# Kernel tuning notes

Hardware: AMD Instinct MI355X
Metric: run time of the kernel (lower is better)

## Reference

```python
import jax, jax.numpy as jnp
import numpy as np

N_REP = 8      # N: repeated gelu(LN(linear)) blocks
M_LAYERS = 4   # M: transformer encoder layers
SEQ = 100
D = 4
FF = 2048      # PyTorch TransformerEncoderLayer default dim_feedforward
H = 4          # nhead; head_dim = 1


def _ln(x, g, b, axes):
    m = jnp.mean(x, axis=axes, keepdims=True)
    v = jnp.var(x, axis=axes, keepdims=True)
    return (x - m) / jnp.sqrt(v + 1e-5) * g + b


def _encoder_layer(x, Win, bi, Wout, bout, W1, b1, W2, b2, g1, be1, g2, be2):
    # x: [S, Nb, D] with S = batch_size (batch_first=False!), Nb = 100
    S, Nb, E = x.shape
    qkv = x @ Win.T + bi                      # [S, Nb, 3D]
    q, k, v = jnp.split(qkv, 3, axis=-1)
    qh = q.reshape(S, Nb, H, E // H)          # head_dim = 1, scale 1/sqrt(1)=1
    kh = k.reshape(S, Nb, H, E // H)
    vh = v.reshape(S, Nb, H, E // H)
    scores = jnp.einsum('snhd,tnhd->nhst', qh, kh)   # [Nb, H, S, S]
    attn = jax.nn.softmax(scores, axis=-1)
    o = jnp.einsum('nhst,tnhd->snhd', attn, vh).reshape(S, Nb, E)
    o = o @ Wout.T + bout
    x = _ln(x + o, g1, be1, (-1,))            # post-norm (norm_first=False)
    f = jax.nn.relu(x @ W1.T + b1) @ W2.T + b2
    return _ln(x + f, g2, be2, (-1,))


def setup_inputs() -> dict:
    key = jax.random.key(0)
    ks = jax.random.split(key, 24)
    B = 256
    d = {}
    d['x'] = jax.random.normal(ks[0], (B, SEQ, D), dtype=jnp.float32)
    # conv1: kernel_size=1, 1->1 channel -> scalar affine
    d['conv_w'] = jax.random.normal(ks[1], (), dtype=jnp.float32) * 0.5 + 1.0
    d['conv_b'] = jax.random.normal(ks[2], (), dtype=jnp.float32) * 0.1
    # shared 4x4 linear (self.liner) and LayerNorm([100,4])
    d['Wl'] = jax.random.normal(ks[3], (D, D), dtype=jnp.float32) * 0.5
    d['bl'] = jax.random.normal(ks[4], (D,), dtype=jnp.float32) * 0.1
    d['ln_g'] = jnp.ones((SEQ, D), dtype=jnp.float32)
    d['ln_b'] = jnp.zeros((SEQ, D), dtype=jnp.float32)
    # transformer encoder params, stacked over M layers
    s = 0.3
    d['Win'] = jax.random.normal(ks[5], (M_LAYERS, 3 * D, D), dtype=jnp.float32) * s
    d['bi'] = jax.random.normal(ks[6], (M_LAYERS, 3 * D), dtype=jnp.float32) * 0.05
    d['Wout'] = jax.random.normal(ks[7], (M_LAYERS, D, D), dtype=jnp.float32) * s
    d['bout'] = jax.random.normal(ks[8], (M_LAYERS, D), dtype=jnp.float32) * 0.05
    d['W1'] = jax.random.normal(ks[9], (M_LAYERS, FF, D), dtype=jnp.float32) * 0.05
    d['b1'] = jax.random.normal(ks[10], (M_LAYERS, FF), dtype=jnp.float32) * 0.05
    d['W2'] = jax.random.normal(ks[11], (M_LAYERS, D, FF), dtype=jnp.float32) * 0.02
    d['b2'] = jax.random.normal(ks[12], (M_LAYERS, D), dtype=jnp.float32) * 0.05
    d['g1'] = jnp.ones((M_LAYERS, D), dtype=jnp.float32)
    d['be1'] = jnp.zeros((M_LAYERS, D), dtype=jnp.float32)
    d['g2'] = jnp.ones((M_LAYERS, D), dtype=jnp.float32)
    d['be2'] = jnp.zeros((M_LAYERS, D), dtype=jnp.float32)
    return d


def reference(x, conv_w, conv_b, Wl, bl, ln_g, ln_b,
              Win, bi, Wout, bout, W1, b1, W2, b2, g1, be1, g2, be2):
    # per-channel kernel_size=1 conv == elementwise affine (same scalar for all 4 channels)
    h = x * conv_w + conv_b                   # [B, 100, 4]
    for _ in range(N_REP):
        h = jax.nn.gelu(_ln(h @ Wl.T + bl, ln_g, ln_b, (-2, -1)), approximate=False)
    h = h @ Wl.T + bl
    for i in range(M_LAYERS):
        h = _encoder_layer(h, Win[i], bi[i], Wout[i], bout[i], W1[i], b1[i],
                           W2[i], b2[i], g1[i], be1[i], g2[i], be2[i])
    h = h @ Wl.T + bl
    return jax.nn.softmax(h, axis=2)
```

## Files before the change

kernel.cpp:

```cpp
#include <hip/hip_runtime.h>
#include <math.h>

#define SEQ   100
#define BATCH 256
#define NREP  8
#define FFD   2048
#define RSQRT2 0.70710678118654752440f

typedef __attribute__((ext_vector_type(16))) float fv16;
typedef __attribute__((ext_vector_type(4)))  float fv4;

__device__ __forceinline__ float wsum(float v) {
#pragma unroll
  for (int o = 32; o > 0; o >>= 1) v += __shfl_xor(v, o, 64);
  return v;
}

__global__ __launch_bounds__(256) void k_prep(
    const float* __restrict__ W1, const float* __restrict__ b1,
    const float* __restrict__ W2, float* __restrict__ Wp)
{
  const int id = blockIdx.x * 256 + threadIdx.x;
  const int l = id >> 9, g = id & 511, f0 = g * 4;
  float* dst = Wp + id * 36;
  const float* w1 = W1 + (l * FFD + f0) * 4;
#pragma unroll
  for (int i = 0; i < 16; ++i) dst[i] = w1[i];
  const float* w2 = W2 + l * 4 * FFD;
#pragma unroll
  for (int f = 0; f < 4; ++f)
#pragma unroll
    for (int d = 0; d < 4; ++d) dst[16 + f * 4 + d] = w2[d * FFD + f0 + f];
  const float* bb = b1 + l * FFD + f0;
#pragma unroll
  for (int f = 0; f < 4; ++f) dst[32 + f] = bb[f];
}

__global__ __launch_bounds__(64) void k_stageA(
    const float* __restrict__ x, const float* __restrict__ convw,
    const float* __restrict__ convb, const float* __restrict__ Wl,
    const float* __restrict__ bl, const float* __restrict__ lng,
    const float* __restrict__ lnb, float* __restrict__ XT)
{
  const int b = blockIdx.x;
  const int lane = threadIdx.x;
  const bool act = lane < 50;

  const float cw = convw[0], cb = convb[0];
  float W[4][4], B[4];
#pragma unroll
  for (int j = 0; j < 4; ++j) {
    B[j] = bl[j];
#pragma unroll
    for (int d = 0; d < 4; ++d) W[j][d] = Wl[j * 4 + d];
  }
  float h[2][4] = {{0.f,0.f,0.f,0.f},{0.f,0.f,0.f,0.f}};
  float gg[2][4] = {{0.f}}, eb[2][4] = {{0.f}};
  if (act) {
#pragma unroll
    for (int p = 0; p < 2; ++p) {
      const int r = lane * 2 + p;
      float4 xr = *(const float4*)(x + (b * SEQ + r) * 4);
      h[p][0] = fmaf(xr.x, cw, cb); h[p][1] = fmaf(xr.y, cw, cb);
      h[p][2] = fmaf(xr.z, cw, cb); h[p][3] = fmaf(xr.w, cw, cb);
      float4 gv = *(const float4*)(lng + r * 4);
      float4 bv = *(const float4*)(lnb + r * 4);
      gg[p][0] = gv.x; gg[p][1] = gv.y; gg[p][2] = gv.z; gg[p][3] = gv.w;
      eb[p][0] = bv.x; eb[p][1] = bv.y; eb[p][2] = bv.z; eb[p][3] = bv.w;
    }
  }
  for (int it = 0; it < NREP; ++it) {
    float y[2][4] = {{0.f,0.f,0.f,0.f},{0.f,0.f,0.f,0.f}};
    float s1 = 0.f, s2 = 0.f;
    if (act) {
#pragma unroll
      for (int p = 0; p < 2; ++p)
#pragma unroll
        for (int j = 0; j < 4; ++j) {
          float yy = B[j];
#pragma unroll
          for (int d = 0; d < 4; ++d) yy = fmaf(h[p][d], W[j][d], yy);
          y[p][j] = yy; s1 += yy; s2 = fmaf(yy, yy, s2);
        }
    }
    s1 = wsum(s1); s2 = wsum(s2);
    const float mean = s1 * (1.0f / 400.0f);
    const float var  = s2 * (1.0f / 400.0f) - mean * mean;
    const float rstd = rsqrtf(var + 1e-5f);
    if (act) {
#pragma unroll
      for (int p = 0; p < 2; ++p)
#pragma unroll
        for (int j = 0; j < 4; ++j) {
          float vv = fmaf((y[p][j] - mean) * rstd, gg[p][j], eb[p][j]);
          h[p][j] = 0.5f * vv * (1.0f + erff(vv * RSQRT2));
        }
    }
  }
  if (act) {
#pragma unroll
    for (int p = 0; p < 2; ++p) {
      const int r = lane * 2 + p;
      float yy[4];
#pragma unroll
      for (int j = 0; j < 4; ++j) {
        float a = B[j];
#pragma unroll
        for (int d = 0; d < 4; ++d) a = fmaf(h[p][d], W[j][d], a);
        yy[j] = a;
      }
      *(float4*)(XT + (r * BATCH + b) * 4) =
          make_float4(yy[0], yy[1], yy[2], yy[3]);
    }
  }
}

__global__ __launch_bounds__(1024, 4) void k_layer(
    const float* __restrict__ XTin, float* __restrict__ XTout,
    const float* __restrict__ Wa,  const float* __restrict__ ba,
    const float* __restrict__ Wo,  const float* __restrict__ bo,
    const float* __restrict__ Wpl, const float* __restrict__ b2l,
    const float* __restrict__ g1l, const float* __restrict__ e1l,
    const float* __restrict__ g2l, const float* __restrict__ e2l,
    const float* __restrict__ Wl,  const float* __restrict__ bl,
    float* __restrict__ out, const int last)
{
  const int n      = blockIdx.x;
  const int base_s = blockIdx.y * 128;
  const int t      = threadIdx.x;
  const int lane   = t & 63;
  const int wv     = t >> 6;
  const int ah     = wv & 3;
  const int kq     = wv >> 2;

  __shared__ __align__(16) float2 kv[4][256];
  __shared__ float2 part[4][128][5];
  __shared__ float  osm[4][128];
  __shared__ float  x1s[128][4];
  __shared__ float  pacc[16][128][4];
  __shared__ float2 kred[4][4];

  {
    const int s = t & 255, hh = t >> 8;
    float4 xr = *(const float4*)(XTin + (n * BATCH + s) * 4);
    const float* wk = Wa + (4 + hh) * 4;
    const float* wp = Wa + (8 + hh) * 4;
    float k = ba[4+hh] + xr.x*wk[0] + xr.y*wk[1] + xr.z*wk[2] + xr.w*wk[3];
    float v = ba[8+hh] + xr.x*wp[0] + xr.y*wp[1] + xr.z*wp[2] + xr.w*wp[3];
    kv[hh][s] = make_float2(k, v);
  }
  float q0, q1;
  {
    const float* wq = Wa + ah * 4;
    float4 xa = *(const float4*)(XTin + (n * BATCH + base_s + 2 * lane) * 4);
    float4 xb = *(const float4*)(XTin + (n * BATCH + base_s + 2 * lane + 1) * 4);
    q0 = ba[ah] + xa.x*wq[0] + xa.y*wq[1] + xa.z*wq[2] + xa.w*wq[3];
    q1 = ba[ah] + xb.x*wq[0] + xb.y*wq[1] + xb.z*wq[2] + xb.w*wq[3];
  }
  __syncthreads();

  {
    float k = kv[ah][kq * 64 + lane].x;
    float mx = k, mn = k;
#pragma unroll
    for (int o = 32; o > 0; o >>= 1) {
      mx = fmaxf(mx, __shfl_xor(mx, o, 64));
      mn = fminf(mn, __shfl_xor(mn, o, 64));
    }
    if (lane == 0) kred[ah][kq] = make_float2(mx, mn);
  }
  __syncthreads();

  {
    const float kmx = fmaxf(fmaxf(kred[ah][0].x, kred[ah][1].x),
                            fmaxf(kred[ah][2].x, kred[ah][3].x));
    const float kmn = fminf(fminf(kred[ah][0].y, kred[ah][1].y),
                            fminf(kred[ah][2].y, kred[ah][3].y));
    const float m0 = (q0 >= 0.f) ? q0 * kmx : q0 * kmn;
    const float m1 = (q1 >= 0.f) ? q1 * kmx : q1 * kmn;
    const int kb = kq * 64;
    float dA = 0.f, nA = 0.f, dB = 0.f, nB = 0.f;
#pragma unroll 4
    for (int i = 0; i < 32; ++i) {
      const int p = ((lane + i) & 31) * 2;
      float4 kk = *(const float4*)&kv[ah][kb + p];
      float pA0 = __expf(fmaf(q0, kk.x, -m0));
      float pA1 = __expf(fmaf(q0, kk.z, -m0));
      float pB0 = __expf(fmaf(q1, kk.x, -m1));
      float pB1 = __expf(fmaf(q1, kk.z, -m1));
      dA += pA0 + pA1; nA = fmaf(pA1, kk.w, fmaf(pA0, kk.y, nA));
      dB += pB0 + pB1; nB = fmaf(pB1, kk.w, fmaf(pB0, kk.y, nB));
    }
    part[ah][2 * lane][kq]     = make_float2(dA, nA);
    part[ah][2 * lane + 1][kq] = make_float2(dB, nB);
  }
  __syncthreads();

  if (t < 512) {
    const int h = t >> 7, qr = t & 127;
    float2 a = part[h][qr][0], b = part[h][qr][1];
    float2 c = part[h][qr][2], d = part[h][qr][3];
    osm[h][qr] = (a.y + b.y + c.y + d.y) / (a.x + b.x + c.x + d.x);
  }
  __syncthreads();

  if (t < 512) {
    const int r = t >> 2, d = t & 3;
    const float o0 = osm[0][r], o1 = osm[1][r], o2 = osm[2][r], o3 = osm[3][r];
    float rr = XTin[(n * BATCH + base_s + r) * 4 + d] + bo[d]
             + o0*Wo[d*4+0] + o1*Wo[d*4+1] + o2*Wo[d*4+2] + o3*Wo[d*4+3];
    float sum = rr + __shfl_xor(rr, 1, 64); sum += __shfl_xor(sum, 2, 64);
    const float mean = 0.25f * sum;
    const float dv = rr - mean;
    float qq = dv * dv;
    float qs = qq + __shfl_xor(qq, 1, 64); qs += __shfl_xor(qs, 2, 64);
    const float rstd = rsqrtf(0.25f * qs + 1e-5f);
    x1s[r][d] = fmaf(dv * rstd, g1l[d], e1l[d]);
  }
  __syncthreads();

  {
    const int wvu = __builtin_amdgcn_readfirstlane(wv);
    const float* gp = Wpl + (size_t)wvu * 1152;
    const float xA0 = x1s[lane][0],    xA1 = x1s[lane][1];
    const float xA2 = x1s[lane][2],    xA3 = x1s[lane][3];
    const float xB0 = x1s[64+lane][0], xB1 = x1s[64+lane][1];
    const float xB2 = x1s[64+lane][2], xB3 = x1s[64+lane][3];
    float aA0=0.f,aA1=0.f,aA2=0.f,aA3=0.f;
    float aB0=0.f,aB1=0.f,aB2=0.f,aB3=0.f;
#pragma unroll
    for (int g = 0; g < 32; ++g) {
      fv16 w1, w2; fv4 bb;
      asm("s_load_dwordx16 %0, %3, %4\n\t"
          "s_load_dwordx16 %1, %3, %5\n\t"
          "s_load_dwordx4  %2, %3, %6\n\t"
          "s_waitcnt lgkmcnt(0)"
          : "=s"(w1), "=s"(w2), "=s"(bb)
          : "s"(gp), "i"(144 * g), "i"(144 * g + 64), "i"(144 * g + 128));
#pragma unroll
      for (int f = 0; f < 4; ++f) {
        const float w10 = w1[f*4+0], w11 = w1[f*4+1];
        const float w12 = w1[f*4+2], w13 = w1[f*4+3];
        const float w20 = w2[f*4+0], w21 = w2[f*4+1];
        const float w22 = w2[f*4+2], w23 = w2[f*4+3];
        const float bf  = bb[f];
        float hA = fmaf(xA3, w13, fmaf(xA2, w12, fmaf(xA1, w11, fmaf(xA0, w10, bf))));
        hA = fmaxf(hA, 0.f);
        aA0 = fmaf(hA, w20, aA0); aA1 = fmaf(hA, w21, aA1);
        aA2 = fmaf(hA, w22, aA2); aA3 = fmaf(hA, w23, aA3);
        float hB = fmaf(xB3, w13, fmaf(xB2, w12, fmaf(xB1, w11, fmaf(xB0, w10, bf))));
        hB = fmaxf(hB, 0.f);
        aB0 = fmaf(hB, w20, aB0); aB1 = fmaf(hB, w21, aB1);
        aB2 = fmaf(hB, w22, aB2); aB3 = fmaf(hB, w23, aB3);
      }
    }
    *(float4*)&pacc[wv][lane][0]      = make_float4(aA0, aA1, aA2, aA3);
    *(float4*)&pacc[wv][64 + lane][0] = make_float4(aB0, aB1, aB2, aB3);
  }
  __syncthreads();

  if (t < 512) {
    const int r = t >> 2, d = t & 3;
    float s16 = b2l[d];
#pragma unroll
    for (int w = 0; w < 16; ++w) s16 += pacc[w][r][d];
    float val = x1s[r][d] + s16;
    float sum = val + __shfl_xor(val, 1, 64); sum += __shfl_xor(sum, 2, 64);
    const float mean = 0.25f * sum;
    const float dv = val - mean;
    float qq = dv * dv;
    float qs = qq + __shfl_xor(qq, 1, 64); qs += __shfl_xor(qs, 2, 64);
    const float rstd = rsqrtf(0.25f * qs + 1e-5f);
    const float res = fmaf(dv * rstd, g2l[d], e2l[d]);
    if (!last) XTout[(n * BATCH + base_s + r) * 4 + d] = res;
    else       x1s[r][d] = res;
  }

  if (last) {
    __syncthreads();
    if (t < 512) {
      const int r = t >> 2, j = t & 3;
      const float y = fmaf(x1s[r][3], Wl[j*4+3], fmaf(x1s[r][2], Wl[j*4+2],
                      fmaf(x1s[r][1], Wl[j*4+1], fmaf(x1s[r][0], Wl[j*4+0], bl[j]))));
      float mx = fmaxf(y, __shfl_xor(y, 1, 64)); mx = fmaxf(mx, __shfl_xor(mx, 2, 64));
      const float e = __expf(y - mx);
      float se = e + __shfl_xor(e, 1, 64); se += __shfl_xor(se, 2, 64);
      out[((base_s + r) * SEQ + n) * 4 + j] = e / se;
    }
  }
}

extern "C" void kernel_launch(void* const* d_in, const int* in_sizes, int n_in,
                              void* d_out, int out_size, void* d_ws, size_t ws_size,
                              hipStream_t stream)
{
  const float* x     = (const float*)d_in[0];
  const float* convw = (const float*)d_in[1];
  const float* convb = (const float*)d_in[2];
  const float* Wl    = (const float*)d_in[3];
  const float* bl    = (const float*)d_in[4];
  const float* lng   = (const float*)d_in[5];
  const float* lnb   = (const float*)d_in[6];
  const float* Win   = (const float*)d_in[7];
  const float* bi    = (const float*)d_in[8];
  const float* Wout  = (const float*)d_in[9];
  const float* bout  = (const float*)d_in[10];
  const float* W1    = (const float*)d_in[11];
  const float* b1    = (const float*)d_in[12];
  const float* W2    = (const float*)d_in[13];
  const float* b2    = (const float*)d_in[14];
  const float* g1    = (const float*)d_in[15];
  const float* be1   = (const float*)d_in[16];
  const float* g2    = (const float*)d_in[17];
  const float* be2   = (const float*)d_in[18];

  float* XT0 = (float*)d_ws;
  float* XT1 = XT0 + SEQ * BATCH * 4;
  float* Wp  = XT1 + SEQ * BATCH * 4;

  k_prep<<<8, 256, 0, stream>>>(W1, b1, W2, Wp);
  k_stageA<<<BATCH, 64, 0, stream>>>(x, convw, convb, Wl, bl, lng, lnb, XT0);
  for (int l = 0; l < 4; ++l) {
    const float* in  = (l & 1) ? XT1 : XT0;
    float*       outb= (l & 1) ? XT0 : XT1;
    k_layer<<<dim3(SEQ, 2), 1024, 0, stream>>>(
        in, outb,
        Win + l * 48, bi + l * 12, Wout + l * 16, bout + l * 4,
        Wp + l * 512 * 36, b2 + l * 4,
        g1 + l * 4, be1 + l * 4, g2 + l * 4, be2 + l * 4,
        Wl, bl, (float*)d_out, (l == 3) ? 1 : 0);
  }
}
```

Measured before the change: 125.8 us.

## Merge prep and stage-A kernels, split layer blocks into 64-query tiles

The weight-repacking kernel and the stage-A kernel are merged into one launch, with the first 8 blocks doing the prep and the rest handling 4 batches each as separate waves. This removes one launch. The layer kernel now uses 512-thread blocks covering 64 queries each, launched on a 100x4 grid instead of 100x2 with 1024 threads. Each wave therefore processes one query row against a 128-key half and 256 FF units instead of two rows. The aim is more, smaller blocks for better occupancy and less reduction work, at the cost of recomputing K/V per block and loading the FFN weights twice as often.

```diff
diff --git a/kernel.cpp b/kernel.cpp
--- a/kernel.cpp
+++ b/kernel.cpp
@@ -16,34 +16,35 @@
   return v;
 }
 
-__global__ __launch_bounds__(256) void k_prep(
+__global__ __launch_bounds__(256) void k_prepA(
     const float* __restrict__ W1, const float* __restrict__ b1,
-    const float* __restrict__ W2, float* __restrict__ Wp)
-{
-  const int id = blockIdx.x * 256 + threadIdx.x;
-  const int l = id >> 9, g = id & 511, f0 = g * 4;
-  float* dst = Wp + id * 36;
-  const float* w1 = W1 + (l * FFD + f0) * 4;
-#pragma unroll
-  for (int i = 0; i < 16; ++i) dst[i] = w1[i];
-  const float* w2 = W2 + l * 4 * FFD;
-#pragma unroll
-  for (int f = 0; f < 4; ++f)
-#pragma unroll
-    for (int d = 0; d < 4; ++d) dst[16 + f * 4 + d] = w2[d * FFD + f0 + f];
-  const float* bb = b1 + l * FFD + f0;
-#pragma unroll
-  for (int f = 0; f < 4; ++f) dst[32 + f] = bb[f];
-}
-
-__global__ __launch_bounds__(64) void k_stageA(
+    const float* __restrict__ W2, float* __restrict__ Wp,
     const float* __restrict__ x, const float* __restrict__ convw,
     const float* __restrict__ convb, const float* __restrict__ Wl,
     const float* __restrict__ bl, const float* __restrict__ lng,
     const float* __restrict__ lnb, float* __restrict__ XT)
 {
-  const int b = blockIdx.x;
-  const int lane = threadIdx.x;
+  const int t = threadIdx.x;
+  if (blockIdx.x < 8) {
+    const int id = blockIdx.x * 256 + t;
+    const int l = id >> 9, g = id & 511, f0 = g * 4;
+    float* dst = Wp + id * 36;
+    const float* w1 = W1 + (l * FFD + f0) * 4;
+#pragma unroll
+    for (int i = 0; i < 16; ++i) dst[i] = w1[i];
+    const float* w2 = W2 + l * 4 * FFD;
+#pragma unroll
+    for (int f = 0; f < 4; ++f)
+#pragma unroll
+      for (int d = 0; d < 4; ++d) dst[16 + f * 4 + d] = w2[d * FFD + f0 + f];
+    const float* bb = b1 + l * FFD + f0;
+#pragma unroll
+    for (int f = 0; f < 4; ++f) dst[32 + f] = bb[f];
+    return;
+  }
+
+  const int b = (blockIdx.x - 8) * 4 + (t >> 6);
+  const int lane = t & 63;
   const bool act = lane < 50;
 
   const float cw = convw[0], cb = convb[0];
@@ -115,7 +116,7 @@
   }
 }
 
-__global__ __launch_bounds__(1024, 4) void k_layer(
+__global__ __launch_bounds__(512, 4) void k_layer(
     const float* __restrict__ XTin, float* __restrict__ XTout,
     const float* __restrict__ Wa,  const float* __restrict__ ba,
     const float* __restrict__ Wo,  const float* __restrict__ bo,
@@ -125,89 +126,88 @@
     const float* __restrict__ Wl,  const float* __restrict__ bl,
     float* __restrict__ out, const int last)
 {
-  const int n      = blockIdx.x;
-  const int base_s = blockIdx.y * 128;
-  const int t      = threadIdx.x;
-  const int lane   = t & 63;
-  const int wv     = t >> 6;
-  const int ah     = wv & 3;
-  const int kq     = wv >> 2;
+  const int n     = blockIdx.x;
+  const int qbase = blockIdx.y * 64;
+  const int t     = threadIdx.x;
+  const int lane  = t & 63;
+  const int wv    = t >> 6;
+  const int ah    = wv & 3;
+  const int kh    = wv >> 2;
 
   __shared__ __align__(16) float2 kv[4][256];
-  __shared__ float2 part[4][128][5];
-  __shared__ float  osm[4][128];
-  __shared__ float  x1s[128][4];
-  __shared__ float  pacc[16][128][4];
-  __shared__ float2 kred[4][4];
-
-  {
-    const int s = t & 255, hh = t >> 8;
+  __shared__ float2 part[4][64][3];
+  __shared__ float  osm[4][64];
+  __shared__ float  x1s[64][4];
+  __shared__ float  pacc[8][64][4];
+  __shared__ float2 kred[4][2];
+
+  {
+    const int s = t & 255, hp = t >> 8;
     float4 xr = *(const float4*)(XTin + (n * BATCH + s) * 4);
-    const float* wk = Wa + (4 + hh) * 4;
-    const float* wp = Wa + (8 + hh) * 4;
-    float k = ba[4+hh] + xr.x*wk[0] + xr.y*wk[1] + xr.z*wk[2] + xr.w*wk[3];
-    float v = ba[8+hh] + xr.x*wp[0] + xr.y*wp[1] + xr.z*wp[2] + xr.w*wp[3];
-    kv[hh][s] = make_float2(k, v);
-  }
-  float q0, q1;
+#pragma unroll
+    for (int i = 0; i < 2; ++i) {
+      const int hh = hp * 2 + i;
+      const float* wk = Wa + (4 + hh) * 4;
+      const float* wp = Wa + (8 + hh) * 4;
+      float k = ba[4+hh] + xr.x*wk[0] + xr.y*wk[1] + xr.z*wk[2] + xr.w*wk[3];
+      float v = ba[8+hh] + xr.x*wp[0] + xr.y*wp[1] + xr.z*wp[2] + xr.w*wp[3];
+      kv[hh][s] = make_float2(k, v);
+    }
+  }
+  float q;
   {
     const float* wq = Wa + ah * 4;
-    float4 xa = *(const float4*)(XTin + (n * BATCH + base_s + 2 * lane) * 4);
-    float4 xb = *(const float4*)(XTin + (n * BATCH + base_s + 2 * lane + 1) * 4);
-    q0 = ba[ah] + xa.x*wq[0] + xa.y*wq[1] + xa.z*wq[2] + xa.w*wq[3];
-    q1 = ba[ah] + xb.x*wq[0] + xb.y*wq[1] + xb.z*wq[2] + xb.w*wq[3];
-  }
-  __syncthreads();
-
-  {
-    float k = kv[ah][kq * 64 + lane].x;
-    float mx = k, mn = k;
+    float4 xa = *(const float4*)(XTin + (n * BATCH + qbase + lane) * 4);
+    q = ba[ah] + xa.x*wq[0] + xa.y*wq[1] + xa.z*wq[2] + xa.w*wq[3];
+  }
+  __syncthreads();
+
+  {
+    float a = kv[ah][kh * 128 + lane].x;
+    float c = kv[ah][kh * 128 + 64 + lane].x;
+    float mx = fmaxf(a, c), mn = fminf(a, c);
 #pragma unroll
     for (int o = 32; o > 0; o >>= 1) {
       mx = fmaxf(mx, __shfl_xor(mx, o, 64));
       mn = fminf(mn, __shfl_xor(mn, o, 64));
     }
-    if (lane == 0) kred[ah][kq] = make_float2(mx, mn);
-  }
-  __syncthreads();
-
-  {
-    const float kmx = fmaxf(fmaxf(kred[ah][0].x, kred[ah][1].x),
-                            fmaxf(kred[ah][2].x, kred[ah][3].x));
-    const float kmn = fminf(fminf(kred[ah][0].y, kred[ah][1].y),
-                            fminf(kred[ah][2].y, kred[ah][3].y));
-    const float m0 = (q0 >= 0.f) ? q0 * kmx : q0 * kmn;
-    const float m1 = (q1 >= 0.f) ? q1 * kmx : q1 * kmn;
-    const int kb = kq * 64;
-    float dA = 0.f, nA = 0.f, dB = 0.f, nB = 0.f;
+    if (lane == 0) kred[ah][kh] = make_float2(mx, mn);
+  }
+  __syncthreads();
+
+  {
+    const float kmx = fmaxf(kred[ah][0].x, kred[ah][1].x);
+    const float kmn = fminf(kred[ah][0].y, kred[ah][1].y);
+    const float m = (q >= 0.f) ? q * kmx : q * kmn;
+    float d0 = 0.f, d1 = 0.f, n0 = 0.f, n1 = 0.f;
+#pragma unroll
+    for (int w = 0; w < 2; ++w) {
+      const int kb = kh * 128 + w * 64;
 #pragma unroll 4
-    for (int i = 0; i < 32; ++i) {
-      const int p = ((lane + i) & 31) * 2;
-      float4 kk = *(const float4*)&kv[ah][kb + p];
-      float pA0 = __expf(fmaf(q0, kk.x, -m0));
-      float pA1 = __expf(fmaf(q0, kk.z, -m0));
-      float pB0 = __expf(fmaf(q1, kk.x, -m1));
-      float pB1 = __expf(fmaf(q1, kk.z, -m1));
-      dA += pA0 + pA1; nA = fmaf(pA1, kk.w, fmaf(pA0, kk.y, nA));
-      dB += pB0 + pB1; nB = fmaf(pB1, kk.w, fmaf(pB0, kk.y, nB));
-    }
-    part[ah][2 * lane][kq]     = make_float2(dA, nA);
-    part[ah][2 * lane + 1][kq] = make_float2(dB, nB);
-  }
-  __syncthreads();
-
-  if (t < 512) {
-    const int h = t >> 7, qr = t & 127;
-    float2 a = part[h][qr][0], b = part[h][qr][1];
-    float2 c = part[h][qr][2], d = part[h][qr][3];
-    osm[h][qr] = (a.y + b.y + c.y + d.y) / (a.x + b.x + c.x + d.x);
-  }
-  __syncthreads();
-
-  if (t < 512) {
+      for (int i = 0; i < 32; ++i) {
+        const int p = ((lane + i) & 31) * 2;
+        float4 kk = *(const float4*)&kv[ah][kb + p];
+        float p0 = __expf(fmaf(q, kk.x, -m));
+        float p1 = __expf(fmaf(q, kk.z, -m));
+        d0 += p0; n0 = fmaf(p0, kk.y, n0);
+        d1 += p1; n1 = fmaf(p1, kk.w, n1);
+      }
+    }
+    part[ah][lane][kh] = make_float2(d0 + d1, n0 + n1);
+  }
+  __syncthreads();
+
+  if (t < 256) {
+    const int h = t >> 6, r = t & 63;
+    float2 a = part[h][r][0], b = part[h][r][1];
+    osm[h][r] = (a.y + b.y) / (a.x + b.x);
+  }
+  __syncthreads();
+
+  if (t < 256) {
     const int r = t >> 2, d = t & 3;
     const float o0 = osm[0][r], o1 = osm[1][r], o2 = osm[2][r], o3 = osm[3][r];
-    float rr = XTin[(n * BATCH + base_s + r) * 4 + d] + bo[d]
+    float rr = XTin[(n * BATCH + qbase + r) * 4 + d] + bo[d]
              + o0*Wo[d*4+0] + o1*Wo[d*4+1] + o2*Wo[d*4+2] + o3*Wo[d*4+3];
     float sum = rr + __shfl_xor(rr, 1, 64); sum += __shfl_xor(sum, 2, 64);
     const float mean = 0.25f * sum;
@@ -221,15 +221,12 @@
 
   {
     const int wvu = __builtin_amdgcn_readfirstlane(wv);
-    const float* gp = Wpl + (size_t)wvu * 1152;
-    const float xA0 = x1s[lane][0],    xA1 = x1s[lane][1];
-    const float xA2 = x1s[lane][2],    xA3 = x1s[lane][3];
-    const float xB0 = x1s[64+lane][0], xB1 = x1s[64+lane][1];
-    const float xB2 = x1s[64+lane][2], xB3 = x1s[64+lane][3];
-    float aA0=0.f,aA1=0.f,aA2=0.f,aA3=0.f;
-    float aB0=0.f,aB1=0.f,aB2=0.f,aB3=0.f;
-#pragma unroll
-    for (int g = 0; g < 32; ++g) {
+    const float* gp = Wpl + (size_t)wvu * 2304;
+    const float x0 = x1s[lane][0], x1 = x1s[lane][1];
+    const float x2 = x1s[lane][2], x3 = x1s[lane][3];
+    float a0 = 0.f, a1 = 0.f, a2 = 0.f, a3 = 0.f;
+#pragma unroll
+    for (int g = 0; g < 64; ++g) {
       fv16 w1, w2; fv4 bb;
       asm("s_load_dwordx16 %0, %3, %4\n\t"
           "s_load_dwordx16 %1, %3, %5\n\t"
@@ -243,28 +240,22 @@
         const float w12 = w1[f*4+2], w13 = w1[f*4+3];
         const float w20 = w2[f*4+0], w21 = w2[f*4+1];
         const float w22 = w2[f*4+2], w23 = w2[f*4+3];
-        const float bf  = bb[f];
-        float hA = fmaf(xA3, w13, fmaf(xA2, w12, fmaf(xA1, w11, fmaf(xA0, w10, bf))));
-        hA = fmaxf(hA, 0.f);
-        aA0 = fmaf(hA, w20, aA0); aA1 = fmaf(hA, w21, aA1);
-        aA2 = fmaf(hA, w22, aA2); aA3 = fmaf(hA, w23, aA3);
-        float hB = fmaf(xB3, w13, fmaf(xB2, w12, fmaf(xB1, w11, fmaf(xB0, w10, bf))));
-        hB = fmaxf(hB, 0.f);
-        aB0 = fmaf(hB, w20, aB0); aB1 = fmaf(hB, w21, aB1);
-        aB2 = fmaf(hB, w22, aB2); aB3 = fmaf(hB, w23, aB3);
+        float hh = fmaf(x3, w13, fmaf(x2, w12, fmaf(x1, w11, fmaf(x0, w10, bb[f]))));
+        hh = fmaxf(hh, 0.f);
+        a0 = fmaf(hh, w20, a0); a1 = fmaf(hh, w21, a1);
+        a2 = fmaf(hh, w22, a2); a3 = fmaf(hh, w23, a3);
       }
     }
-    *(float4*)&pacc[wv][lane][0]      = make_float4(aA0, aA1, aA2, aA3);
-    *(float4*)&pacc[wv][64 + lane][0] = make_float4(aB0, aB1, aB2, aB3);
-  }
-  __syncthreads();
-
-  if (t < 512) {
+    *(float4*)&pacc[wv][lane][0] = make_float4(a0, a1, a2, a3);
+  }
+  __syncthreads();
+
+  if (t < 256) {
     const int r = t >> 2, d = t & 3;
-    float s16 = b2l[d];
-#pragma unroll
-    for (int w = 0; w < 16; ++w) s16 += pacc[w][r][d];
-    float val = x1s[r][d] + s16;
+    float s8 = b2l[d];
+#pragma unroll
+    for (int w = 0; w < 8; ++w) s8 += pacc[w][r][d];
+    float val = x1s[r][d] + s8;
     float sum = val + __shfl_xor(val, 1, 64); sum += __shfl_xor(sum, 2, 64);
     const float mean = 0.25f * sum;
     const float dv = val - mean;
@@ -272,20 +263,20 @@
     float qs = qq + __shfl_xor(qq, 1, 64); qs += __shfl_xor(qs, 2, 64);
     const float rstd = rsqrtf(0.25f * qs + 1e-5f);
     const float res = fmaf(dv * rstd, g2l[d], e2l[d]);
-    if (!last) XTout[(n * BATCH + base_s + r) * 4 + d] = res;
+    if (!last) XTout[(n * BATCH + qbase + r) * 4 + d] = res;
     else       x1s[r][d] = res;
   }
 
   if (last) {
     __syncthreads();
-    if (t < 512) {
+    if (t < 256) {
       const int r = t >> 2, j = t & 3;
       const float y = fmaf(x1s[r][3], Wl[j*4+3], fmaf(x1s[r][2], Wl[j*4+2],
                       fmaf(x1s[r][1], Wl[j*4+1], fmaf(x1s[r][0], Wl[j*4+0], bl[j]))));
       float mx = fmaxf(y, __shfl_xor(y, 1, 64)); mx = fmaxf(mx, __shfl_xor(mx, 2, 64));
       const float e = __expf(y - mx);
       float se = e + __shfl_xor(e, 1, 64); se += __shfl_xor(se, 2, 64);
-      out[((base_s + r) * SEQ + n) * 4 + j] = e / se;
+      out[((qbase + r) * SEQ + n) * 4 + j] = e / se;
     }
   }
 }
@@ -318,12 +309,12 @@
   float* XT1 = XT0 + SEQ * BATCH * 4;
   float* Wp  = XT1 + SEQ * BATCH * 4;
 
-  k_prep<<<8, 256, 0, stream>>>(W1, b1, W2, Wp);
-  k_stageA<<<BATCH, 64, 0, stream>>>(x, convw, convb, Wl, bl, lng, lnb, XT0);
+  k_prepA<<<72, 256, 0, stream>>>(W1, b1, W2, Wp,
+                                  x, convw, convb, Wl, bl, lng, lnb, XT0);
   for (int l = 0; l < 4; ++l) {
     const float* in  = (l & 1) ? XT1 : XT0;
     float*       outb= (l & 1) ? XT0 : XT1;
-    k_layer<<<dim3(SEQ, 2), 1024, 0, stream>>>(
+    k_layer<<<dim3(SEQ, 4), 512, 0, stream>>>(
         in, outb,
         Win + l * 48, bi + l * 12, Wout + l * 16, bout + l * 4,
         Wp + l * 512 * 36, b2 + l * 4,
```

After: 133.9 us. 1.06x slower.

## Merge prep and stage-A kernels; halve layer block size to 512 threads

Applied to the files above, without the earlier changes.

Folds the weight-repack kernel and the stage-A kernel into one launch, with the first 8 blocks doing the repack and the rest processing 4 batches each, which removes one kernel launch. The layer kernel drops from 1024 to 512 threads. Each thread now computes one query over all 256 keys instead of two queries over a key quarter, which removes the partial-sum reduction and one barrier. Each FFN wave now covers twice as many hidden units. This trades less cross-wave reduction and sync for longer serial loops per thread and fewer waves per block to hide latency.

```diff
diff --git a/kernel.cpp b/kernel.cpp
--- a/kernel.cpp
+++ b/kernel.cpp
@@ -16,34 +16,35 @@
   return v;
 }
 
-__global__ __launch_bounds__(256) void k_prep(
+__global__ __launch_bounds__(256) void k_prepA(
     const float* __restrict__ W1, const float* __restrict__ b1,
-    const float* __restrict__ W2, float* __restrict__ Wp)
-{
-  const int id = blockIdx.x * 256 + threadIdx.x;
-  const int l = id >> 9, g = id & 511, f0 = g * 4;
-  float* dst = Wp + id * 36;
-  const float* w1 = W1 + (l * FFD + f0) * 4;
-#pragma unroll
-  for (int i = 0; i < 16; ++i) dst[i] = w1[i];
-  const float* w2 = W2 + l * 4 * FFD;
-#pragma unroll
-  for (int f = 0; f < 4; ++f)
-#pragma unroll
-    for (int d = 0; d < 4; ++d) dst[16 + f * 4 + d] = w2[d * FFD + f0 + f];
-  const float* bb = b1 + l * FFD + f0;
-#pragma unroll
-  for (int f = 0; f < 4; ++f) dst[32 + f] = bb[f];
-}
-
-__global__ __launch_bounds__(64) void k_stageA(
+    const float* __restrict__ W2, float* __restrict__ Wp,
     const float* __restrict__ x, const float* __restrict__ convw,
     const float* __restrict__ convb, const float* __restrict__ Wl,
     const float* __restrict__ bl, const float* __restrict__ lng,
     const float* __restrict__ lnb, float* __restrict__ XT)
 {
-  const int b = blockIdx.x;
-  const int lane = threadIdx.x;
+  const int t = threadIdx.x;
+  if (blockIdx.x < 8) {
+    const int id = blockIdx.x * 256 + t;
+    const int l = id >> 9, g = id & 511, f0 = g * 4;
+    float* dst = Wp + id * 36;
+    const float* w1 = W1 + (l * FFD + f0) * 4;
+#pragma unroll
+    for (int i = 0; i < 16; ++i) dst[i] = w1[i];
+    const float* w2 = W2 + l * 4 * FFD;
+#pragma unroll
+    for (int f = 0; f < 4; ++f)
+#pragma unroll
+      for (int d = 0; d < 4; ++d) dst[16 + f * 4 + d] = w2[d * FFD + f0 + f];
+    const float* bb = b1 + l * FFD + f0;
+#pragma unroll
+    for (int f = 0; f < 4; ++f) dst[32 + f] = bb[f];
+    return;
+  }
+
+  const int b = (blockIdx.x - 8) * 4 + (t >> 6);
+  const int lane = t & 63;
   const bool act = lane < 50;
 
   const float cw = convw[0], cb = convb[0];
@@ -115,7 +116,7 @@
   }
 }
 
-__global__ __launch_bounds__(1024, 4) void k_layer(
+__global__ __launch_bounds__(512, 4) void k_layer(
     const float* __restrict__ XTin, float* __restrict__ XTout,
     const float* __restrict__ Wa,  const float* __restrict__ ba,
     const float* __restrict__ Wo,  const float* __restrict__ bo,
@@ -130,81 +131,71 @@
   const int t      = threadIdx.x;
   const int lane   = t & 63;
   const int wv     = t >> 6;
-  const int ah     = wv & 3;
-  const int kq     = wv >> 2;
 
   __shared__ __align__(16) float2 kv[4][256];
-  __shared__ float2 part[4][128][5];
   __shared__ float  osm[4][128];
   __shared__ float  x1s[128][4];
-  __shared__ float  pacc[16][128][4];
-  __shared__ float2 kred[4][4];
-
-  {
-    const int s = t & 255, hh = t >> 8;
+  __shared__ float  pacc[8][128][4];
+  __shared__ float2 kred[4][2];
+
+  {
+    const int s = t & 255, hp = t >> 8;
     float4 xr = *(const float4*)(XTin + (n * BATCH + s) * 4);
-    const float* wk = Wa + (4 + hh) * 4;
-    const float* wp = Wa + (8 + hh) * 4;
-    float k = ba[4+hh] + xr.x*wk[0] + xr.y*wk[1] + xr.z*wk[2] + xr.w*wk[3];
-    float v = ba[8+hh] + xr.x*wp[0] + xr.y*wp[1] + xr.z*wp[2] + xr.w*wp[3];
-    kv[hh][s] = make_float2(k, v);
-  }
-  float q0, q1;
-  {
-    const float* wq = Wa + ah * 4;
-    float4 xa = *(const float4*)(XTin + (n * BATCH + base_s + 2 * lane) * 4);
-    float4 xb = *(const float4*)(XTin + (n * BATCH + base_s + 2 * lane + 1) * 4);
-    q0 = ba[ah] + xa.x*wq[0] + xa.y*wq[1] + xa.z*wq[2] + xa.w*wq[3];
-    q1 = ba[ah] + xb.x*wq[0] + xb.y*wq[1] + xb.z*wq[2] + xb.w*wq[3];
-  }
-  __syncthreads();
-
-  {
-    float k = kv[ah][kq * 64 + lane].x;
-    float mx = k, mn = k;
+#pragma unroll
+    for (int i = 0; i < 2; ++i) {
+      const int hh = hp * 2 + i;
+      const float* wk = Wa + (4 + hh) * 4;
+      const float* wp = Wa + (8 + hh) * 4;
+      float k = ba[4+hh] + xr.x*wk[0] + xr.y*wk[1] + xr.z*wk[2] + xr.w*wk[3];
+      float v = ba[8+hh] + xr.x*wp[0] + xr.y*wp[1] + xr.z*wp[2] + xr.w*wp[3];
+      kv[hh][s] = make_float2(k, v);
+    }
+  }
+  __syncthreads();
+
+  {
+    const int h = wv & 3, strip = wv >> 2;
+    float a = kv[h][strip * 128 + lane].x;
+    float c = kv[h][strip * 128 + 64 + lane].x;
+    float mx = fmaxf(a, c), mn = fminf(a, c);
 #pragma unroll
     for (int o = 32; o > 0; o >>= 1) {
       mx = fmaxf(mx, __shfl_xor(mx, o, 64));
       mn = fminf(mn, __shfl_xor(mn, o, 64));
     }
-    if (lane == 0) kred[ah][kq] = make_float2(mx, mn);
-  }
-  __syncthreads();
-
-  {
-    const float kmx = fmaxf(fmaxf(kred[ah][0].x, kred[ah][1].x),
-                            fmaxf(kred[ah][2].x, kred[ah][3].x));
-    const float kmn = fminf(fminf(kred[ah][0].y, kred[ah][1].y),
-                            fminf(kred[ah][2].y, kred[ah][3].y));
-    const float m0 = (q0 >= 0.f) ? q0 * kmx : q0 * kmn;
-    const float m1 = (q1 >= 0.f) ? q1 * kmx : q1 * kmn;
-    const int kb = kq * 64;
-    float dA = 0.f, nA = 0.f, dB = 0.f, nB = 0.f;
+    if (lane == 0) kred[h][strip] = make_float2(mx, mn);
+  }
+  __syncthreads();
+
+  {
+    const int h = t >> 7, qr = t & 127;
+    const float* wq = Wa + h * 4;
+    float4 xa = *(const float4*)(XTin + (n * BATCH + base_s + qr) * 4);
+    const float q = ba[h] + xa.x*wq[0] + xa.y*wq[1] + xa.z*wq[2] + xa.w*wq[3];
+    const float kmx = fmaxf(kred[h][0].x, kred[h][1].x);
+    const float kmn = fminf(kred[h][0].y, kred[h][1].y);
+    const float m = (q >= 0.f) ? q * kmx : q * kmn;
+    float d0=0.f,d1=0.f,d2=0.f,d3=0.f,n0=0.f,n1=0.f,n2=0.f,n3=0.f;
 #pragma unroll 4
-    for (int i = 0; i < 32; ++i) {
-      const int p = ((lane + i) & 31) * 2;
-      float4 kk = *(const float4*)&kv[ah][kb + p];
-      float pA0 = __expf(fmaf(q0, kk.x, -m0));
-      float pA1 = __expf(fmaf(q0, kk.z, -m0));
-      float pB0 = __expf(fmaf(q1, kk.x, -m1));
-      float pB1 = __expf(fmaf(q1, kk.z, -m1));
-      dA += pA0 + pA1; nA = fmaf(pA1, kk.w, fmaf(pA0, kk.y, nA));
-      dB += pB0 + pB1; nB = fmaf(pB1, kk.w, fmaf(pB0, kk.y, nB));
-    }
-    part[ah][2 * lane][kq]     = make_float2(dA, nA);
-    part[ah][2 * lane + 1][kq] = make_float2(dB, nB);
-  }
-  __syncthreads();
-
-  if (t < 512) {
-    const int h = t >> 7, qr = t & 127;
-    float2 a = part[h][qr][0], b = part[h][qr][1];
-    float2 c = part[h][qr][2], d = part[h][qr][3];
-    osm[h][qr] = (a.y + b.y + c.y + d.y) / (a.x + b.x + c.x + d.x);
-  }
-  __syncthreads();
-
-  if (t < 512) {
+    for (int i = 0; i < 128; i += 2) {
+      const int p0i = (i + lane) & 127;
+      const int p1i = (i + 1 + lane) & 127;
+      float4 a = *(const float4*)&kv[h][p0i * 2];
+      float4 b = *(const float4*)&kv[h][p1i * 2];
+      float pA = __expf(fmaf(q, a.x, -m));
+      float pB = __expf(fmaf(q, a.z, -m));
+      float pC = __expf(fmaf(q, b.x, -m));
+      float pD = __expf(fmaf(q, b.z, -m));
+      d0 += pA; n0 = fmaf(pA, a.y, n0);
+      d1 += pB; n1 = fmaf(pB, a.w, n1);
+      d2 += pC; n2 = fmaf(pC, b.y, n2);
+      d3 += pD; n3 = fmaf(pD, b.w, n3);
+    }
+    osm[h][qr] = (n0 + n1 + n2 + n3) / (d0 + d1 + d2 + d3);
+  }
+  __syncthreads();
+
+  {
     const int r = t >> 2, d = t & 3;
     const float o0 = osm[0][r], o1 = osm[1][r], o2 = osm[2][r], o3 = osm[3][r];
     float rr = XTin[(n * BATCH + base_s + r) * 4 + d] + bo[d]
@@ -221,7 +212,7 @@
 
   {
     const int wvu = __builtin_amdgcn_readfirstlane(wv);
-    const float* gp = Wpl + (size_t)wvu * 1152;
+    const float* gp = Wpl + (size_t)wvu * 2304;
     const float xA0 = x1s[lane][0],    xA1 = x1s[lane][1];
     const float xA2 = x1s[lane][2],    xA3 = x1s[lane][3];
     const float xB0 = x1s[64+lane][0], xB1 = x1s[64+lane][1];
@@ -229,7 +220,7 @@
     float aA0=0.f,aA1=0.f,aA2=0.f,aA3=0.f;
     float aB0=0.f,aB1=0.f,aB2=0.f,aB3=0.f;
 #pragma unroll
-    for (int g = 0; g < 32; ++g) {
+    for (int g = 0; g < 64; ++g) {
       fv16 w1, w2; fv4 bb;
       asm("s_load_dwordx16 %0, %3, %4\n\t"
           "s_load_dwordx16 %1, %3, %5\n\t"
@@ -259,12 +250,12 @@
   }
   __syncthreads();
 
-  if (t < 512) {
+  {
     const int r = t >> 2, d = t & 3;
-    float s16 = b2l[d];
-#pragma unroll
-    for (int w = 0; w < 16; ++w) s16 += pacc[w][r][d];
-    float val = x1s[r][d] + s16;
+    float s8 = b2l[d];
+#pragma unroll
+    for (int w = 0; w < 8; ++w) s8 += pacc[w][r][d];
+    float val = x1s[r][d] + s8;
     float sum = val + __shfl_xor(val, 1, 64); sum += __shfl_xor(sum, 2, 64);
     const float mean = 0.25f * sum;
     const float dv = val - mean;
@@ -278,15 +269,13 @@
 
   if (last) {
     __syncthreads();
-    if (t < 512) {
-      const int r = t >> 2, j = t & 3;
-      const float y = fmaf(x1s[r][3], Wl[j*4+3], fmaf(x1s[r][2], Wl[j*4+2],
-                      fmaf(x1s[r][1], Wl[j*4+1], fmaf(x1s[r][0], Wl[j*4+0], bl[j]))));
-      float mx = fmaxf(y, __shfl_xor(y, 1, 64)); mx = fmaxf(mx, __shfl_xor(mx, 2, 64));
-      const float e = __expf(y - mx);
-      float se = e + __shfl_xor(e, 1, 64); se += __shfl_xor(se, 2, 64);
-      out[((base_s + r) * SEQ + n) * 4 + j] = e / se;
-    }
+    const int r = t >> 2, j = t & 3;
+    const float y = fmaf(x1s[r][3], Wl[j*4+3], fmaf(x1s[r][2], Wl[j*4+2],
+                    fmaf(x1s[r][1], Wl[j*4+1], fmaf(x1s[r][0], Wl[j*4+0], bl[j]))));
+    float mx = fmaxf(y, __shfl_xor(y, 1, 64)); mx = fmaxf(mx, __shfl_xor(mx, 2, 64));
+    const float e = __expf(y - mx);
+    float se = e + __shfl_xor(e, 1, 64); se += __shfl_xor(se, 2, 64);
+    out[((base_s + r) * SEQ + n) * 4 + j] = e / se;
   }
 }
 
@@ -318,12 +307,12 @@
   float* XT1 = XT0 + SEQ * BATCH * 4;
   float* Wp  = XT1 + SEQ * BATCH * 4;
 
-  k_prep<<<8, 256, 0, stream>>>(W1, b1, W2, Wp);
-  k_stageA<<<BATCH, 64, 0, stream>>>(x, convw, convb, Wl, bl, lng, lnb, XT0);
+  k_prepA<<<72, 256, 0, stream>>>(W1, b1, W2, Wp,
+                                  x, convw, convb, Wl, bl, lng, lnb, XT0);
   for (int l = 0; l < 4; ++l) {
     const float* in  = (l & 1) ? XT1 : XT0;
     float*       outb= (l & 1) ? XT0 : XT1;
-    k_layer<<<dim3(SEQ, 2), 1024, 0, stream>>>(
+    k_layer<<<dim3(SEQ, 2), 512, 0, stream>>>(
         in, outb,
         Win + l * 48, bi + l * 12, Wout + l * 16, bout + l * 4,
         Wp + l * 512 * 36, b2 + l * 4,
```

After: 150.5 us. +19.6%, slower.
